# Optimization experiments

Measured on AMD Instinct MI355X. Metric: run time of the kernel, lower is better.

The kernel has to match this reference:

```python
import jax, jax.numpy as jnp
import numpy as np
from jax import lax

B, T, V, E, H, F = 128, 32, 32000, 128, 256, 2048


def setup_inputs() -> dict:
    key = jax.random.key(0)
    ks = jax.random.split(key, 20)
    s = 0.02
    return {
        "features": jax.random.normal(ks[0], (B, F), jnp.float32),
        "captions": jax.random.randint(ks[1], (B, T), 0, V),
        "embeddings": jax.random.normal(ks[2], (V, E), jnp.float32) * s,
        "W_ih": jax.random.normal(ks[3], (4 * H, E + F), jnp.float32) * s,
        "b_ih": jnp.zeros((4 * H,), jnp.float32),
        "W_hh": jax.random.normal(ks[4], (4 * H, H), jnp.float32) * s,
        "b_hh": jnp.zeros((4 * H,), jnp.float32),
        "fc_W": jax.random.normal(ks[5], (H, V), jnp.float32) * s,
        "fc_b": jnp.zeros((V,), jnp.float32),
        "Wa_W": jax.random.normal(ks[6], (F, H), jnp.float32) * s,
        "Wa_b": jnp.zeros((H,), jnp.float32),
        "Ua_W": jax.random.normal(ks[7], (H, H), jnp.float32) * s,
        "Ua_b": jnp.zeros((H,), jnp.float32),
        "va_W": jax.random.normal(ks[8], (H, 1), jnp.float32) * s,
        "va_b": jnp.zeros((1,), jnp.float32),
        "initH_W": jax.random.normal(ks[9], (F, H), jnp.float32) * s,
        "initH_b": jnp.zeros((H,), jnp.float32),
        "initC_W": jax.random.normal(ks[10], (F, H), jnp.float32) * s,
        "initC_b": jnp.zeros((H,), jnp.float32),
    }


def reference(features, captions, embeddings, W_ih, b_ih, W_hh, b_hh, fc_W, fc_b,
              Wa_W, Wa_b, Ua_W, Ua_b, va_W, va_b, initH_W, initH_b, initC_W, initC_b):
    feats = features[:, None, :]                     # [B,1,F]
    mean_ann = jnp.mean(feats, axis=1)               # [B,F]
    h0 = mean_ann @ initH_W + initH_b                # [B,H]
    c0 = mean_ann @ initC_W + initC_b
    embed = embeddings[captions]                     # [B,T,E] teacher forcing
    atten1 = feats @ Wa_W + Wa_b                     # [B,1,H] (loop-invariant)

    def step(carry, word_embed):
        h, c = carry
        atten2 = (h @ Ua_W + Ua_b)[:, None, :]       # [B,1,H]
        score = jnp.tanh(atten1 + atten2) @ va_W + va_b  # [B,1,1]
        w = jax.nn.softmax(score, axis=1)
        context = jnp.sum(w * feats, axis=1)         # [B,F]
        x = jnp.concatenate([word_embed, context], axis=1)  # [B,E+F]
        gates = x @ W_ih.T + b_ih + h @ W_hh.T + b_hh       # [B,4H]
        i, f, g, o = jnp.split(gates, 4, axis=1)     # PyTorch LSTMCell gate order
        i = jax.nn.sigmoid(i)
        f = jax.nn.sigmoid(f)
        g = jnp.tanh(g)
        o = jax.nn.sigmoid(o)
        c_new = f * c + i * g
        h_new = o * jnp.tanh(c_new)                  # dropout = identity (eval)
        out = h_new @ fc_W + fc_b                    # [B,V]
        return (h_new, c_new), out

    _, outs = lax.scan(step, (h0, c0), jnp.swapaxes(embed, 0, 1))  # [T,B,V]
    return jnp.swapaxes(outs, 0, 1)                  # [B,T,V]
```

## Files before the change

### kernel.cpp

```cpp
#include <hip/hip_runtime.h>
#include <stdint.h>

#define B_   128
#define T_   32
#define V_   32000
#define E_   128
#define H_   256
#define F_   2048
#define G4   1024
#define EF   2176

typedef __attribute__((ext_vector_type(8))) short bh8;
typedef __attribute__((ext_vector_type(4))) short bh4;
typedef __attribute__((ext_vector_type(4))) float floatx4;

__device__ __forceinline__ short f2bf(float f) {
    union { float f; uint32_t u; } v; v.f = f;
    uint32_t r = (v.u + 0x7fffu + ((v.u >> 16) & 1u)) >> 16;
    return (short)(uint16_t)r;
}

__global__ __launch_bounds__(256) void cvt_f2b(
    const float* __restrict__ in, short* __restrict__ out)
{
    const size_t i = (size_t)blockIdx.x * 256 + threadIdx.x;
    const floatx4 v = *(const floatx4*)&in[i * 4];
    bh4 o;
    o[0] = f2bf(v[0]); o[1] = f2bf(v[1]); o[2] = f2bf(v[2]); o[3] = f2bf(v[3]);
    *(bh4*)&out[i * 4] = o;
}

__global__ __launch_bounds__(256) void transpose_f2b(
    const float* __restrict__ in, short* __restrict__ out, int R, int C)
{
    __shared__ float tile[64][68];
    const int c0 = blockIdx.x * 64, r0 = blockIdx.y * 64;
    const int x = threadIdx.x & 15, y = threadIdx.x >> 4;
#pragma unroll
    for (int i = 0; i < 4; i++) {
        const int r = y + i * 16;
        *(floatx4*)&tile[r][x * 4] = *(const floatx4*)&in[(size_t)(r0 + r) * C + c0 + x * 4];
    }
    __syncthreads();
#pragma unroll
    for (int i = 0; i < 4; i++) {
        const int cc = y + i * 16;
        bh4 v;
        v[0] = f2bf(tile[x * 4 + 0][cc]);
        v[1] = f2bf(tile[x * 4 + 1][cc]);
        v[2] = f2bf(tile[x * 4 + 2][cc]);
        v[3] = f2bf(tile[x * 4 + 3][cc]);
        *(bh4*)&out[(size_t)(c0 + cc) * R + r0 + x * 4] = v;
    }
}

__global__ __launch_bounds__(256) void gather_embed(
    const int* __restrict__ captions, const float* __restrict__ emb,
    short* __restrict__ out)
{
    const int r = blockIdx.x * 16 + (threadIdx.x >> 4);
    const int chunk = threadIdx.x & 15;
    const int t = r >> 7, b = r & 127;
    const int cap = captions[b * T_ + t];
    const floatx4* src = (const floatx4*)&emb[(size_t)cap * E_];
    const floatx4 a = src[chunk * 2], c = src[chunk * 2 + 1];
    bh8 o;
    o[0] = f2bf(a[0]); o[1] = f2bf(a[1]); o[2] = f2bf(a[2]); o[3] = f2bf(a[3]);
    o[4] = f2bf(c[0]); o[5] = f2bf(c[1]); o[6] = f2bf(c[2]); o[7] = f2bf(c[3]);
    ((bh8*)out)[(size_t)r * 16 + chunk] = o;
}

#define TM 128
#define TN 128
#define BKG 64

__global__ __launch_bounds__(256) void gemm_nt(
    const short* __restrict__ A, int lda,
    const short* __restrict__ B, int ldb,
    int K,
    float* __restrict__ Cf, short* __restrict__ Cb, int ldc,
    const float* __restrict__ bias1, const float* __restrict__ bias2)
{
    __shared__ short As[TM * BKG];
    __shared__ short Bs[TN * BKG];
    const int tid  = threadIdx.x;
    const int lane = tid & 63, quad = lane >> 4, l15 = lane & 15;
    const int wv   = tid >> 6;
    const int wr   = wv >> 1, wc = wv & 1;
    const short* Ab = A + (size_t)blockIdx.y * TM * lda;
    const short* Bb = B + (size_t)blockIdx.x * TN * ldb;
    const int srow = tid >> 3;
    const int skof = (tid & 7) << 3;

    floatx4 zero = {0.f, 0.f, 0.f, 0.f};
    floatx4 acc[4][4];
#pragma unroll
    for (int i = 0; i < 4; i++)
#pragma unroll
        for (int j = 0; j < 4; j++) acc[i][j] = zero;

    for (int k0 = 0; k0 < K; k0 += BKG) {
        __syncthreads();
#pragma unroll
        for (int j = 0; j < 4; j++) {
            const int r = j * 32 + srow;
            *(bh8*)&As[r * BKG + skof] = *(const bh8*)&Ab[(size_t)r * lda + k0 + skof];
            *(bh8*)&Bs[r * BKG + skof] = *(const bh8*)&Bb[(size_t)r * ldb + k0 + skof];
        }
        __syncthreads();
#pragma unroll
        for (int ks = 0; ks < 2; ks++) {
            bh8 af[4], bfr[4];
#pragma unroll
            for (int i = 0; i < 4; i++)
                af[i] = *(const bh8*)&As[(wr * 64 + i * 16 + l15) * BKG + ks * 32 + quad * 8];
#pragma unroll
            for (int j = 0; j < 4; j++)
                bfr[j] = *(const bh8*)&Bs[(wc * 64 + j * 16 + l15) * BKG + ks * 32 + quad * 8];
#pragma unroll
            for (int i = 0; i < 4; i++)
#pragma unroll
                for (int j = 0; j < 4; j++)
                    acc[i][j] = __builtin_amdgcn_mfma_f32_16x16x32_bf16(af[i], bfr[j], acc[i][j], 0, 0, 0);
        }
    }

#pragma unroll
    for (int i = 0; i < 4; i++) {
        const int m = blockIdx.y * TM + wr * 64 + i * 16 + quad * 4;
#pragma unroll
        for (int j = 0; j < 4; j++) {
            const int n = blockIdx.x * TN + wc * 64 + j * 16 + l15;
            float bias = 0.f;
            if (bias1) bias += bias1[n];
            if (bias2) bias += bias2[n];
#pragma unroll
            for (int r = 0; r < 4; r++) {
                const float v = acc[i][j][r] + bias;
                if (Cf) Cf[(size_t)(m + r) * ldc + n] = v;
                else    Cb[(size_t)(m + r) * ldc + n] = f2bf(v);
            }
        }
    }
}

#define RBLK 32

__device__ __forceinline__ void gridbar(unsigned* bar) {
    __syncthreads();
    __threadfence();
    if (threadIdx.x == 0) {
        const unsigned g   = __hip_atomic_load(&bar[1], __ATOMIC_RELAXED, __HIP_MEMORY_SCOPE_AGENT);
        const unsigned old = __hip_atomic_fetch_add(&bar[0], 1u, __ATOMIC_ACQ_REL, __HIP_MEMORY_SCOPE_AGENT);
        if (old == RBLK - 1) {
            __hip_atomic_store(&bar[0], 0u, __ATOMIC_RELAXED, __HIP_MEMORY_SCOPE_AGENT);
            __hip_atomic_store(&bar[1], g + 1u, __ATOMIC_RELEASE, __HIP_MEMORY_SCOPE_AGENT);
        } else {
            while (__hip_atomic_load(&bar[1], __ATOMIC_ACQUIRE, __HIP_MEMORY_SCOPE_AGENT) == g)
                __builtin_amdgcn_s_sleep(1);
        }
    }
    __syncthreads();
    __threadfence();
}

__global__ __launch_bounds__(256) void recurrence(
    const short* __restrict__ Whh,
    const short* __restrict__ Wih,
    const float* __restrict__ fg,
    const short* __restrict__ embB,
    short* h0buf,
    short* h1buf,
    const float* __restrict__ c0,
    short* __restrict__ Hall,
    unsigned* bar)
{
    __shared__ short Ws[32 * 256];
    __shared__ short We[32 * 128];
    __shared__ float Gs[128 * 32];
    const int tid  = threadIdx.x;
    const int lane = tid & 63, quad = lane >> 4, l15 = lane & 15, wv = tid >> 6;
    const int u0   = blockIdx.x * 8;

    {
        const int q = tid >> 3;
        const int col = (q >> 3) * H_ + u0 + (q & 7);
        {
            const int ko = (tid & 7) * 32;
            const bh8* src = (const bh8*)&Whh[(size_t)col * H_ + ko];
            bh8* dst = (bh8*)&Ws[q * 256 + ko];
#pragma unroll
            for (int i = 0; i < 4; i++) dst[i] = src[i];
        }
        {
            const int ko = (tid & 7) * 16;
            const bh8* src = (const bh8*)&Wih[(size_t)col * EF + ko];
            bh8* dst = (bh8*)&We[q * 128 + ko];
            dst[0] = src[0]; dst[1] = src[1];
        }
    }

    const int uu = tid & 7, bb = tid >> 3;
    float c[4];
#pragma unroll
    for (int k = 0; k < 4; k++) c[k] = c0[(bb + 32 * k) * H_ + u0 + uu];
    __syncthreads();

    for (int t = 0; t < T_; t++) {
        const short* hr = (t & 1) ? h1buf : h0buf;
        short*       hw = (t & 1) ? h0buf : h1buf;
        const short* et = embB + (size_t)t * B_ * E_;

        floatx4 zero = {0.f, 0.f, 0.f, 0.f};
        floatx4 acc[2][2];
#pragma unroll
        for (int i = 0; i < 2; i++)
#pragma unroll
            for (int j = 0; j < 2; j++) acc[i][j] = zero;

#pragma unroll
        for (int s = 0; s < 8; s++) {
            bh8 af[2], bfr[2];
#pragma unroll
            for (int i = 0; i < 2; i++)
                af[i] = *(const bh8*)&hr[(wv * 32 + i * 16 + l15) * H_ + s * 32 + quad * 8];
#pragma unroll
            for (int j = 0; j < 2; j++)
                bfr[j] = *(const bh8*)&Ws[(j * 16 + l15) * 256 + s * 32 + quad * 8];
#pragma unroll
            for (int i = 0; i < 2; i++)
#pragma unroll
                for (int j = 0; j < 2; j++)
                    acc[i][j] = __builtin_amdgcn_mfma_f32_16x16x32_bf16(af[i], bfr[j], acc[i][j], 0, 0, 0);
        }
#pragma unroll
        for (int s = 0; s < 4; s++) {
            bh8 af[2], bfr[2];
#pragma unroll
            for (int i = 0; i < 2; i++)
                af[i] = *(const bh8*)&et[(wv * 32 + i * 16 + l15) * E_ + s * 32 + quad * 8];
#pragma unroll
            for (int j = 0; j < 2; j++)
                bfr[j] = *(const bh8*)&We[(j * 16 + l15) * 128 + s * 32 + quad * 8];
#pragma unroll
            for (int i = 0; i < 2; i++)
#pragma unroll
                for (int j = 0; j < 2; j++)
                    acc[i][j] = __builtin_amdgcn_mfma_f32_16x16x32_bf16(af[i], bfr[j], acc[i][j], 0, 0, 0);
        }
#pragma unroll
        for (int i = 0; i < 2; i++)
#pragma unroll
            for (int j = 0; j < 2; j++)
#pragma unroll
                for (int r = 0; r < 4; r++)
                    Gs[(wv * 32 + i * 16 + quad * 4 + r) * 32 + j * 16 + l15] = acc[i][j][r];
        __syncthreads();

#pragma unroll
        for (int k = 0; k < 4; k++) {
            const int b     = bb + 32 * k;
            const int gbase = b * G4 + u0 + uu;
            const float xi = Gs[b * 32 + uu]      + fg[gbase];
            const float xf = Gs[b * 32 + 8 + uu]  + fg[gbase + 256];
            const float xg = Gs[b * 32 + 16 + uu] + fg[gbase + 512];
            const float xo = Gs[b * 32 + 24 + uu] + fg[gbase + 768];
            const float ig  = 1.f / (1.f + __expf(-xi));
            const float fgt = 1.f / (1.f + __expf(-xf));
            const float gg  = tanhf(xg);
            const float og  = 1.f / (1.f + __expf(-xo));
            c[k] = fgt * c[k] + ig * gg;
            const float h = og * tanhf(c[k]);
            const short hb = f2bf(h);
            hw[b * H_ + u0 + uu] = hb;
            Hall[(size_t)(b * T_ + t) * H_ + u0 + uu] = hb;
        }
        if (t < T_ - 1) gridbar(bar);
    }
}

extern "C" void kernel_launch(void* const* d_in, const int* in_sizes, int n_in,
                              void* d_out, int out_size, void* d_ws, size_t ws_size,
                              hipStream_t stream)
{
    (void)in_sizes; (void)n_in; (void)out_size; (void)ws_size;
    const float* features   = (const float*)d_in[0];
    const int*   captions   = (const int*)  d_in[1];
    const float* embeddings = (const float*)d_in[2];
    const float* W_ih       = (const float*)d_in[3];
    const float* b_ih       = (const float*)d_in[4];
    const float* W_hh       = (const float*)d_in[5];
    const float* b_hh       = (const float*)d_in[6];
    const float* fc_W       = (const float*)d_in[7];
    const float* fc_b       = (const float*)d_in[8];
    const float* initH_W    = (const float*)d_in[15];
    const float* initH_b    = (const float*)d_in[16];
    const float* initC_W    = (const float*)d_in[17];
    const float* initC_b    = (const float*)d_in[18];
    float* out = (float*)d_out;

    char* ws = (char*)d_ws;
    size_t off = 0;
    auto alloc = [&](size_t bytes) -> void* {
        void* p = ws + off; off += (bytes + 255) & ~(size_t)255; return p;
    };
    unsigned* bar = (unsigned*)alloc(256);
    short* featB  = (short*)alloc((size_t)B_ * F_ * 2);
    short* WihB   = (short*)alloc((size_t)G4 * EF * 2);
    short* WhhB   = (short*)alloc((size_t)G4 * H_ * 2);
    short* fcWt   = (short*)alloc((size_t)V_ * H_ * 2);
    short* iHt    = (short*)alloc((size_t)H_ * F_ * 2);
    short* iCt    = (short*)alloc((size_t)H_ * F_ * 2);
    short* embB   = (short*)alloc((size_t)B_ * T_ * E_ * 2);
    float* fg     = (float*)alloc((size_t)B_ * G4 * 4);
    short* h0buf  = (short*)alloc((size_t)B_ * H_ * 2);
    short* h1buf  = (short*)alloc((size_t)B_ * H_ * 2);
    float* c0f    = (float*)alloc((size_t)B_ * H_ * 4);
    short* Hall   = (short*)alloc((size_t)B_ * T_ * H_ * 2);

    hipMemsetAsync(bar, 0, 256, stream);

    cvt_f2b<<<dim3(B_ * F_ / 1024), 256, 0, stream>>>(features, featB);
    cvt_f2b<<<dim3(G4 * EF / 1024), 256, 0, stream>>>(W_ih, WihB);
    cvt_f2b<<<dim3(G4 * H_ / 1024), 256, 0, stream>>>(W_hh, WhhB);
    transpose_f2b<<<dim3(V_ / 64, H_ / 64), 256, 0, stream>>>(fc_W, fcWt, H_, V_);
    transpose_f2b<<<dim3(H_ / 64, F_ / 64), 256, 0, stream>>>(initH_W, iHt, F_, H_);
    transpose_f2b<<<dim3(H_ / 64, F_ / 64), 256, 0, stream>>>(initC_W, iCt, F_, H_);
    gather_embed<<<dim3(B_ * T_ / 16), 256, 0, stream>>>(captions, embeddings, embB);

    gemm_nt<<<dim3(H_ / TN, 1), 256, 0, stream>>>(featB, F_, iHt, F_, F_,
                                                  nullptr, h0buf, H_, initH_b, nullptr);
    gemm_nt<<<dim3(H_ / TN, 1), 256, 0, stream>>>(featB, F_, iCt, F_, F_,
                                                  c0f, nullptr, H_, initC_b, nullptr);
    gemm_nt<<<dim3(G4 / TN, 1), 256, 0, stream>>>(featB, F_, WihB + E_, EF, F_,
                                                  fg, nullptr, G4, b_ih, b_hh);
    recurrence<<<dim3(RBLK), 256, 0, stream>>>(WhhB, WihB, fg, embB,
                                               h0buf, h1buf, c0f, Hall, bar);
    gemm_nt<<<dim3(V_ / TN, B_ * T_ / TM), 256, 0, stream>>>(Hall, H_, fcWt, H_, H_,
                                                             out, nullptr, V_, fc_b, nullptr);
}
```

Measured before the change: 1.210 ms.

## Batch-partition LSTM recurrence to drop grid barriers; hoist embedding gate GEMM

The recurrence is split by batch instead of hidden unit, so each of 32 blocks owns 4 batch rows and all 1024 gates. Hidden state stays in LDS and the cross-block grid barrier is gone. The embedding part of the input projection moves out of the loop into one large GEMM. The three init GEMMs merge into one launch, GEMM tile loads switch to direct global-to-LDS loads, and the workspace for the fc weight transpose is aliased with the gate buffer. The cost is that every block streams the full W_hh from global or L2 on each step, and MFMA rows are wasted because only 4 of the 16 batch rows are real.

```diff
diff --git a/kernel.cpp b/kernel.cpp
--- a/kernel.cpp
+++ b/kernel.cpp
@@ -13,6 +13,9 @@
 typedef __attribute__((ext_vector_type(8))) short bh8;
 typedef __attribute__((ext_vector_type(4))) short bh4;
 typedef __attribute__((ext_vector_type(4))) float floatx4;
+
+typedef __attribute__((address_space(1))) const void gv_t;
+typedef __attribute__((address_space(3))) void lv_t;
 
 __device__ __forceinline__ short f2bf(float f) {
     union { float f; uint32_t u; } v; v.f = f;
@@ -74,21 +77,20 @@
 #define TN 128
 #define BKG 64
 
-__global__ __launch_bounds__(256) void gemm_nt(
+__device__ __forceinline__ void gemm_body(
     const short* __restrict__ A, int lda,
     const short* __restrict__ B, int ldb,
     int K,
     float* __restrict__ Cf, short* __restrict__ Cb, int ldc,
-    const float* __restrict__ bias1, const float* __restrict__ bias2)
-{
-    __shared__ short As[TM * BKG];
-    __shared__ short Bs[TN * BKG];
+    const float* __restrict__ bias1, const float* __restrict__ bias2,
+    int bx, int by, short* As, short* Bs)
+{
     const int tid  = threadIdx.x;
     const int lane = tid & 63, quad = lane >> 4, l15 = lane & 15;
     const int wv   = tid >> 6;
     const int wr   = wv >> 1, wc = wv & 1;
-    const short* Ab = A + (size_t)blockIdx.y * TM * lda;
-    const short* Bb = B + (size_t)blockIdx.x * TN * ldb;
+    const short* Ab = A + (size_t)by * TM * lda;
+    const short* Bb = B + (size_t)bx * TN * ldb;
     const int srow = tid >> 3;
     const int skof = (tid & 7) << 3;
 
@@ -104,8 +106,12 @@
 #pragma unroll
         for (int j = 0; j < 4; j++) {
             const int r = j * 32 + srow;
-            *(bh8*)&As[r * BKG + skof] = *(const bh8*)&Ab[(size_t)r * lda + k0 + skof];
-            *(bh8*)&Bs[r * BKG + skof] = *(const bh8*)&Bb[(size_t)r * ldb + k0 + skof];
+            __builtin_amdgcn_global_load_lds(
+                (gv_t*)&Ab[(size_t)r * lda + k0 + skof],
+                (lv_t*)&As[(j * 32 + wv * 8) * BKG], 16, 0, 0);
+            __builtin_amdgcn_global_load_lds(
+                (gv_t*)&Bb[(size_t)r * ldb + k0 + skof],
+                (lv_t*)&Bs[(j * 32 + wv * 8) * BKG], 16, 0, 0);
         }
         __syncthreads();
 #pragma unroll
@@ -127,10 +133,10 @@
 
 #pragma unroll
     for (int i = 0; i < 4; i++) {
-        const int m = blockIdx.y * TM + wr * 64 + i * 16 + quad * 4;
+        const int m = by * TM + wr * 64 + i * 16 + quad * 4;
 #pragma unroll
         for (int j = 0; j < 4; j++) {
-            const int n = blockIdx.x * TN + wc * 64 + j * 16 + l15;
+            const int n = bx * TN + wc * 64 + j * 16 + l15;
             float bias = 0.f;
             if (bias1) bias += bias1[n];
             if (bias2) bias += bias2[n];
@@ -144,138 +150,124 @@
     }
 }
 
-#define RBLK 32
-
-__device__ __forceinline__ void gridbar(unsigned* bar) {
-    __syncthreads();
-    __threadfence();
-    if (threadIdx.x == 0) {
-        const unsigned g   = __hip_atomic_load(&bar[1], __ATOMIC_RELAXED, __HIP_MEMORY_SCOPE_AGENT);
-        const unsigned old = __hip_atomic_fetch_add(&bar[0], 1u, __ATOMIC_ACQ_REL, __HIP_MEMORY_SCOPE_AGENT);
-        if (old == RBLK - 1) {
-            __hip_atomic_store(&bar[0], 0u, __ATOMIC_RELAXED, __HIP_MEMORY_SCOPE_AGENT);
-            __hip_atomic_store(&bar[1], g + 1u, __ATOMIC_RELEASE, __HIP_MEMORY_SCOPE_AGENT);
-        } else {
-            while (__hip_atomic_load(&bar[1], __ATOMIC_ACQUIRE, __HIP_MEMORY_SCOPE_AGENT) == g)
-                __builtin_amdgcn_s_sleep(1);
-        }
-    }
-    __syncthreads();
-    __threadfence();
-}
-
-__global__ __launch_bounds__(256) void recurrence(
+__global__ __launch_bounds__(256) void gemm_nt(
+    const short* __restrict__ A, int lda,
+    const short* __restrict__ B, int ldb, int K,
+    float* __restrict__ Cf, short* __restrict__ Cb, int ldc,
+    const float* __restrict__ bias1, const float* __restrict__ bias2)
+{
+    __shared__ short As[TM * BKG];
+    __shared__ short Bs[TN * BKG];
+    gemm_body(A, lda, B, ldb, K, Cf, Cb, ldc, bias1, bias2,
+              blockIdx.x, blockIdx.y, As, Bs);
+}
+
+__global__ __launch_bounds__(256) void init_gemms(
+    const short* __restrict__ featB, const short* __restrict__ iHt,
+    const short* __restrict__ iCt, const short* __restrict__ WihB,
+    short* __restrict__ h0, float* __restrict__ c0, float* __restrict__ fg,
+    const float* __restrict__ initH_b, const float* __restrict__ initC_b,
+    const float* __restrict__ b_ih, const float* __restrict__ b_hh)
+{
+    __shared__ short As[TM * BKG];
+    __shared__ short Bs[TN * BKG];
+    const int bid = blockIdx.x;
+    if (bid < 2)
+        gemm_body(featB, F_, iHt, F_, F_, nullptr, h0, H_, initH_b, nullptr, bid, 0, As, Bs);
+    else if (bid < 4)
+        gemm_body(featB, F_, iCt, F_, F_, c0, nullptr, H_, initC_b, nullptr, bid - 2, 0, As, Bs);
+    else
+        gemm_body(featB, F_, WihB + E_, EF, F_, fg, nullptr, G4, b_ih, b_hh, bid - 4, 0, As, Bs);
+}
+
+#define HS 272
+
+__global__ __launch_bounds__(256, 1) void recurrence2(
     const short* __restrict__ Whh,
-    const short* __restrict__ Wih,
     const float* __restrict__ fg,
-    const short* __restrict__ embB,
-    short* h0buf,
-    short* h1buf,
+    const float* __restrict__ eg,
+    const short* __restrict__ h0,
     const float* __restrict__ c0,
-    short* __restrict__ Hall,
-    unsigned* bar)
-{
-    __shared__ short Ws[32 * 256];
-    __shared__ short We[32 * 128];
-    __shared__ float Gs[128 * 32];
+    short* __restrict__ Hall)
+{
+    __shared__ short hs[16 * HS];
+    __shared__ float fgs[4 * G4];
+    __shared__ float Gs[4 * G4];
     const int tid  = threadIdx.x;
     const int lane = tid & 63, quad = lane >> 4, l15 = lane & 15, wv = tid >> 6;
-    const int u0   = blockIdx.x * 8;
-
-    {
-        const int q = tid >> 3;
-        const int col = (q >> 3) * H_ + u0 + (q & 7);
-        {
-            const int ko = (tid & 7) * 32;
-            const bh8* src = (const bh8*)&Whh[(size_t)col * H_ + ko];
-            bh8* dst = (bh8*)&Ws[q * 256 + ko];
-#pragma unroll
-            for (int i = 0; i < 4; i++) dst[i] = src[i];
-        }
-        {
-            const int ko = (tid & 7) * 16;
-            const bh8* src = (const bh8*)&Wih[(size_t)col * EF + ko];
-            bh8* dst = (bh8*)&We[q * 128 + ko];
-            dst[0] = src[0]; dst[1] = src[1];
-        }
-    }
-
-    const int uu = tid & 7, bb = tid >> 3;
+    const int b0   = blockIdx.x * 4;
+    const int u    = tid;
+
+#pragma unroll
+    for (int i = 0; i < 16; i++) {
+        const int idx = tid + i * 256;
+        fgs[idx] = fg[(size_t)(b0 + (idx >> 10)) * G4 + (idx & 1023)];
+    }
+#pragma unroll
+    for (int b = 0; b < 4; b++)
+        hs[b * HS + tid] = h0[(size_t)(b0 + b) * H_ + tid];
+#pragma unroll
+    for (int rr = 4; rr < 16; rr++)
+        hs[rr * HS + tid] = 0;
     float c[4];
 #pragma unroll
-    for (int k = 0; k < 4; k++) c[k] = c0[(bb + 32 * k) * H_ + u0 + uu];
+    for (int b = 0; b < 4; b++) c[b] = c0[(size_t)(b0 + b) * H_ + u];
     __syncthreads();
 
+    const floatx4 zero = {0.f, 0.f, 0.f, 0.f};
     for (int t = 0; t < T_; t++) {
-        const short* hr = (t & 1) ? h1buf : h0buf;
-        short*       hw = (t & 1) ? h0buf : h1buf;
-        const short* et = embB + (size_t)t * B_ * E_;
-
-        floatx4 zero = {0.f, 0.f, 0.f, 0.f};
-        floatx4 acc[2][2];
-#pragma unroll
-        for (int i = 0; i < 2; i++)
-#pragma unroll
-            for (int j = 0; j < 2; j++) acc[i][j] = zero;
-
-#pragma unroll
-        for (int s = 0; s < 8; s++) {
-            bh8 af[2], bfr[2];
-#pragma unroll
-            for (int i = 0; i < 2; i++)
-                af[i] = *(const bh8*)&hr[(wv * 32 + i * 16 + l15) * H_ + s * 32 + quad * 8];
-#pragma unroll
-            for (int j = 0; j < 2; j++)
-                bfr[j] = *(const bh8*)&Ws[(j * 16 + l15) * 256 + s * 32 + quad * 8];
-#pragma unroll
-            for (int i = 0; i < 2; i++)
-#pragma unroll
-                for (int j = 0; j < 2; j++)
-                    acc[i][j] = __builtin_amdgcn_mfma_f32_16x16x32_bf16(af[i], bfr[j], acc[i][j], 0, 0, 0);
-        }
-#pragma unroll
-        for (int s = 0; s < 4; s++) {
-            bh8 af[2], bfr[2];
-#pragma unroll
-            for (int i = 0; i < 2; i++)
-                af[i] = *(const bh8*)&et[(wv * 32 + i * 16 + l15) * E_ + s * 32 + quad * 8];
-#pragma unroll
-            for (int j = 0; j < 2; j++)
-                bfr[j] = *(const bh8*)&We[(j * 16 + l15) * 128 + s * 32 + quad * 8];
-#pragma unroll
-            for (int i = 0; i < 2; i++)
-#pragma unroll
-                for (int j = 0; j < 2; j++)
-                    acc[i][j] = __builtin_amdgcn_mfma_f32_16x16x32_bf16(af[i], bfr[j], acc[i][j], 0, 0, 0);
-        }
-#pragma unroll
-        for (int i = 0; i < 2; i++)
-#pragma unroll
-            for (int j = 0; j < 2; j++)
+        float egv[4][4];
+#pragma unroll
+        for (int b = 0; b < 4; b++)
+#pragma unroll
+            for (int g = 0; g < 4; g++)
+                egv[b][g] = eg[(size_t)(t * B_ + b0 + b) * G4 + g * H_ + u];
+
+        bh8 af[8];
+#pragma unroll
+        for (int s = 0; s < 8; s++)
+            af[s] = *(const bh8*)&hs[l15 * HS + s * 32 + quad * 8];
+
+        floatx4 acc[16];
+#pragma unroll
+        for (int j = 0; j < 16; j++) acc[j] = zero;
+#pragma unroll
+        for (int j = 0; j < 16; j++) {
+            const short* wrow = &Whh[(size_t)(wv * 256 + j * 16 + l15) * H_ + quad * 8];
+#pragma unroll
+            for (int s = 0; s < 8; s++)
+                acc[j] = __builtin_amdgcn_mfma_f32_16x16x32_bf16(
+                    af[s], *(const bh8*)&wrow[s * 32], acc[j], 0, 0, 0);
+        }
+
+        if (quad == 0) {
+#pragma unroll
+            for (int j = 0; j < 16; j++) {
+                const int col = wv * 256 + j * 16 + l15;
 #pragma unroll
                 for (int r = 0; r < 4; r++)
-                    Gs[(wv * 32 + i * 16 + quad * 4 + r) * 32 + j * 16 + l15] = acc[i][j][r];
+                    Gs[r * G4 + col] = acc[j][r];
+            }
+        }
         __syncthreads();
 
 #pragma unroll
-        for (int k = 0; k < 4; k++) {
-            const int b     = bb + 32 * k;
-            const int gbase = b * G4 + u0 + uu;
-            const float xi = Gs[b * 32 + uu]      + fg[gbase];
-            const float xf = Gs[b * 32 + 8 + uu]  + fg[gbase + 256];
-            const float xg = Gs[b * 32 + 16 + uu] + fg[gbase + 512];
-            const float xo = Gs[b * 32 + 24 + uu] + fg[gbase + 768];
+        for (int b = 0; b < 4; b++) {
+            const float xi = Gs[b * G4 + u]          + fgs[b * G4 + u]          + egv[b][0];
+            const float xf = Gs[b * G4 + H_ + u]     + fgs[b * G4 + H_ + u]     + egv[b][1];
+            const float xg = Gs[b * G4 + 2 * H_ + u] + fgs[b * G4 + 2 * H_ + u] + egv[b][2];
+            const float xo = Gs[b * G4 + 3 * H_ + u] + fgs[b * G4 + 3 * H_ + u] + egv[b][3];
             const float ig  = 1.f / (1.f + __expf(-xi));
             const float fgt = 1.f / (1.f + __expf(-xf));
             const float gg  = tanhf(xg);
             const float og  = 1.f / (1.f + __expf(-xo));
-            c[k] = fgt * c[k] + ig * gg;
-            const float h = og * tanhf(c[k]);
+            c[b] = fgt * c[b] + ig * gg;
+            const float h = og * tanhf(c[b]);
             const short hb = f2bf(h);
-            hw[b * H_ + u0 + uu] = hb;
-            Hall[(size_t)(b * T_ + t) * H_ + u0 + uu] = hb;
-        }
-        if (t < T_ - 1) gridbar(bar);
+            hs[b * HS + u] = hb;
+            Hall[(size_t)((b0 + b) * T_ + t) * H_ + u] = hb;
+        }
+        __syncthreads();
     }
 }
 
@@ -304,38 +296,35 @@
     auto alloc = [&](size_t bytes) -> void* {
         void* p = ws + off; off += (bytes + 255) & ~(size_t)255; return p;
     };
-    unsigned* bar = (unsigned*)alloc(256);
+    void*  X      = alloc((size_t)B_ * T_ * G4 * 4);
+    float* eg     = (float*)X;
+    short* fcWt   = (short*)X;
     short* featB  = (short*)alloc((size_t)B_ * F_ * 2);
     short* WihB   = (short*)alloc((size_t)G4 * EF * 2);
     short* WhhB   = (short*)alloc((size_t)G4 * H_ * 2);
-    short* fcWt   = (short*)alloc((size_t)V_ * H_ * 2);
     short* iHt    = (short*)alloc((size_t)H_ * F_ * 2);
     short* iCt    = (short*)alloc((size_t)H_ * F_ * 2);
     short* embB   = (short*)alloc((size_t)B_ * T_ * E_ * 2);
     float* fg     = (float*)alloc((size_t)B_ * G4 * 4);
     short* h0buf  = (short*)alloc((size_t)B_ * H_ * 2);
-    short* h1buf  = (short*)alloc((size_t)B_ * H_ * 2);
     float* c0f    = (float*)alloc((size_t)B_ * H_ * 4);
     short* Hall   = (short*)alloc((size_t)B_ * T_ * H_ * 2);
-
-    hipMemsetAsync(bar, 0, 256, stream);
 
     cvt_f2b<<<dim3(B_ * F_ / 1024), 256, 0, stream>>>(features, featB);
     cvt_f2b<<<dim3(G4 * EF / 1024), 256, 0, stream>>>(W_ih, WihB);
     cvt_f2b<<<dim3(G4 * H_ / 1024), 256, 0, stream>>>(W_hh, WhhB);
-    transpose_f2b<<<dim3(V_ / 64, H_ / 64), 256, 0, stream>>>(fc_W, fcWt, H_, V_);
     transpose_f2b<<<dim3(H_ / 64, F_ / 64), 256, 0, stream>>>(initH_W, iHt, F_, H_);
     transpose_f2b<<<dim3(H_ / 64, F_ / 64), 256, 0, stream>>>(initC_W, iCt, F_, H_);
     gather_embed<<<dim3(B_ * T_ / 16), 256, 0, stream>>>(captions, embeddings, embB);
 
-    gemm_nt<<<dim3(H_ / TN, 1), 256, 0, stream>>>(featB, F_, iHt, F_, F_,
-                                                  nullptr, h0buf, H_, initH_b, nullptr);
-    gemm_nt<<<dim3(H_ / TN, 1), 256, 0, stream>>>(featB, F_, iCt, F_, F_,
-                                                  c0f, nullptr, H_, initC_b, nullptr);
-    gemm_nt<<<dim3(G4 / TN, 1), 256, 0, stream>>>(featB, F_, WihB + E_, EF, F_,
-                                                  fg, nullptr, G4, b_ih, b_hh);
-    recurrence<<<dim3(RBLK), 256, 0, stream>>>(WhhB, WihB, fg, embB,
-                                               h0buf, h1buf, c0f, Hall, bar);
+    init_gemms<<<dim3(12), 256, 0, stream>>>(featB, iHt, iCt, WihB,
+                                             h0buf, c0f, fg,
+                                             initH_b, initC_b, b_ih, b_hh);
+    gemm_nt<<<dim3(G4 / TN, B_ * T_ / TM), 256, 0, stream>>>(embB, E_, WihB, EF, E_,
+                                                             eg, nullptr, G4, nullptr, nullptr);
+    recurrence2<<<dim3(32), 256, 0, stream>>>(WhhB, fg, eg, h0buf, c0f, Hall);
+
+    transpose_f2b<<<dim3(V_ / 64, H_ / 64), 256, 0, stream>>>(fc_W, fcWt, H_, V_);
     gemm_nt<<<dim3(V_ / TN, B_ * T_ / TM), 256, 0, stream>>>(Hall, H_, fcWt, H_, H_,
                                                              out, nullptr, V_, fc_b, nullptr);
 }
```

After: 998.1 us. 17.5% less time.
